# Optimization experiments

Hardware: AMD Instinct MI355X
Metric: run time of the kernel (lower is better)

The kernel has to match this reference:

```python
import jax, jax.numpy as jnp
import numpy as np

B, T, L, A, O = 16, 32, 64, 64, 16
EL, EA, EO = 128, 128, 128
FL, FA, FO, C = 256, 256, 256, 768


def setup_inputs() -> dict:
    key = jax.random.key(0)
    ks = jax.random.split(key, 16)
    s = 0.02
    return {
        "lab_feats": jax.random.normal(ks[0], (B, T, L, FL), jnp.float32),
        "abn_feats": jax.random.normal(ks[1], (B, T, A, FA), jnp.float32),
        "lab_concept_emb": jax.random.normal(ks[2], (L, C), jnp.float32),
        "abn_concept_emb": jax.random.normal(ks[3], (A, C), jnp.float32),
        "lab_rel_emb": jax.random.normal(ks[4], (EL, C), jnp.float32),
        "abn_rel_emb": jax.random.normal(ks[5], (EA, C), jnp.float32),
        "W_lab": jax.random.normal(ks[6], (FL + C, FL), jnp.float32) * s,
        "b_lab": jnp.zeros((FL,), jnp.float32),
        "W_abn": jax.random.normal(ks[7], (FA + C, FA), jnp.float32) * s,
        "b_abn": jnp.zeros((FA,), jnp.float32),
        "W_org": jax.random.normal(ks[8], (FL, FO), jnp.float32) * s,
        "b_org": jnp.zeros((FO,), jnp.float32),
        "D": jax.random.normal(ks[9], (C, FL), jnp.float32) * s,
        "W_o2a": jax.random.normal(ks[10], (FO, FA), jnp.float32) * s,
        "b_o2a": jnp.zeros((FA,), jnp.float32),
        "time_mask": jnp.ones((B, T), dtype=bool),
        "lab_idx": jax.random.randint(ks[11], (EL,), 0, L),
        "lab_org_idx": jax.random.randint(ks[12], (EL,), 0, O),
        "abn_idx": jax.random.randint(ks[13], (EA,), 0, A),
        "abn_org_idx": jax.random.randint(ks[14], (EA,), 0, O),
        "o2a_abn_idx": jax.random.randint(ks[15], (EO,), 0, A),
        "o2a_org_idx": jax.random.randint(jax.random.fold_in(key, 99), (EO,), 0, O),
        "num_organs": O,
    }


def _scatter_mean(attended, org_idx, num_organs, time_mask):
    # attended: (B,T,E,F); emulate legacy per-edge accumulate: cnt[o] = deg(o)*w(b,t)
    onehot = (org_idx[:, None] == jnp.arange(num_organs)[None, :]).astype(attended.dtype)  # (E,O)
    sum_o = jnp.einsum('btef,eo->btof', attended, onehot)
    deg = onehot.sum(0)                                    # (O,)
    w = time_mask.astype(attended.dtype)                   # (B,T)
    cnt = w[:, :, None] * deg[None, None, :]               # (B,T,O)
    mean_o = sum_o / jnp.maximum(cnt, 1e-9)[..., None]
    return mean_o, cnt > 0


def reference(lab_feats, abn_feats, lab_concept_emb, abn_concept_emb,
              lab_rel_emb, abn_rel_emb, W_lab, b_lab, W_abn, b_abn,
              W_org, b_org, D, W_o2a, b_o2a,
              time_mask, lab_idx, lab_org_idx, abn_idx, abn_org_idx,
              o2a_abn_idx, o2a_org_idx, num_organs):
    Fl = lab_feats.shape[-1]
    Fa = abn_feats.shape[-1]
    A_ = abn_feats.shape[2]

    # --- lab -> organ: gather, concat(feat, concept+relation), W_lab (split to avoid concat) ---
    x = lab_feats[:, :, lab_idx, :]                        # (B,T,El,Fl)
    c = lab_concept_emb[lab_idx] + lab_rel_emb             # (El,C)
    h = jnp.tanh(jnp.einsum('btef,fg->bteg', x, W_lab[:Fl]) + c @ W_lab[Fl:] + b_lab)
    attended = h + lab_rel_emb @ D                         # relation-projection D
    mean_lab, mask_lab = _scatter_mean(attended, lab_org_idx, num_organs, time_mask)

    # --- abn -> organ ---
    xa = abn_feats[:, :, abn_idx, :]
    ca = abn_concept_emb[abn_idx] + abn_rel_emb
    ha = jnp.tanh(jnp.einsum('btef,fg->bteg', xa, W_abn[:Fa]) + ca @ W_abn[Fa:] + b_abn)
    mean_abn, mask_abn = _scatter_mean(ha, abn_org_idx, num_organs, time_mask)

    # --- organ states ---
    organ_states = jnp.tanh(jnp.einsum('btof,fg->btog', mean_lab + mean_abn, W_org) + b_org)
    organ_states = organ_states * (mask_lab | mask_abn)[..., None].astype(organ_states.dtype)

    # --- organ -> abnormality message passing (mean over incident organs) ---
    msg = jnp.einsum('btog,gf->btof', organ_states, W_o2a) + b_o2a   # (B,T,O,Fa)
    gathered = msg[:, :, o2a_org_idx, :]                   # (B,T,Eo,Fa)
    onehot = (o2a_abn_idx[:, None] == jnp.arange(A_)[None, :]).astype(msg.dtype)  # (Eo,A)
    agg = jnp.einsum('btef,ea->btaf', gathered, onehot)
    deg = jnp.maximum(onehot.sum(0), 1.0)                  # (A,)
    abn_out = abn_feats + agg / deg[None, None, :, None]
    return abn_out
```

## Files before the change

kernel.cpp:

```cpp
#include <hip/hip_runtime.h>
#include <math.h>

#define NBT 512
#define NF  256
#define NC  768
#define NROW 64
#define NORG 16
#define NE  128
#define SLD 260
#define SY  264

#define WS_SW_LAB1 0
#define WS_SW_ABN1 131072
#define WS_SW_ORG  1441792
#define WS_SW_O2A  1572864
#define WS_SUMREL  1703936
#define WS_LAB_CB  1753088
#define WS_ABN_CB  1884160
#define WS_ADDSUM  2015232
#define WS_WCNT    2031616
#define WS_INVL    2035712
#define WS_INVA    2035776
#define WS_MASK    2035840
#define WS_SRTL    2035904
#define WS_SRTA    2036544
#define WS_RAWL    2097152
#define WS_RAWA    10485760
#define WS_NEED    18874368

typedef __attribute__((ext_vector_type(8)))  short bf16x8;
typedef __attribute__((ext_vector_type(16))) float f32x16;
typedef __attribute__((ext_vector_type(4)))  float f32x4;

__device__ __forceinline__ short f2bf(float f) {
    union { float f; unsigned u; } v; v.f = f;
    unsigned r = v.u + 0x7FFF + ((v.u >> 16) & 1);
    return (short)(r >> 16);
}
__device__ __forceinline__ float bf2f(short s) {
    return __uint_as_float(((unsigned)(unsigned short)s) << 16);
}
__device__ __forceinline__ float tanh_fast(float x) {
    float xc = fminf(fmaxf(x, -15.f), 15.f);
    float e = __expf(2.f * xc);
    return 1.f - 2.f * __builtin_amdgcn_rcpf(e + 1.f);
}
__device__ __forceinline__ f32x16 mfma32(bf16x8 a, bf16x8 b, f32x16 c) {
    return __builtin_amdgcn_mfma_f32_32x32x16_bf16(a, b, c, 0, 0, 0);
}
__device__ __forceinline__ f32x4 mfma16(bf16x8 a, bf16x8 b, f32x4 c) {
    return __builtin_amdgcn_mfma_f32_16x16x32_bf16(a, b, c, 0, 0, 0);
}
__device__ __forceinline__ bf16x8 pack_a16(const float* __restrict__ p) {
    float4 x0 = *(const float4*)p;
    float4 x1 = *(const float4*)(p + 4);
    union { bf16x8 v; unsigned u[4]; } r;
    r.u[0] = __builtin_amdgcn_perm(__float_as_uint(x0.y), __float_as_uint(x0.x), 0x07060302);
    r.u[1] = __builtin_amdgcn_perm(__float_as_uint(x0.w), __float_as_uint(x0.z), 0x07060302);
    r.u[2] = __builtin_amdgcn_perm(__float_as_uint(x1.y), __float_as_uint(x1.x), 0x07060302);
    r.u[3] = __builtin_amdgcn_perm(__float_as_uint(x1.w), __float_as_uint(x1.z), 0x07060302);
    return r.v;
}

__device__ __forceinline__ void swz32(const float* __restrict__ src, short* __restrict__ dst, int s) {
    const int l = s & 63, rest = s >> 6;
    const int nt = rest & 7, k16 = rest >> 3;
    const int n = nt * 32 + (l & 31);
    const int kb = k16 * 16 + ((l >> 5) & 1) * 8;
    bf16x8 v;
    #pragma unroll
    for (int j = 0; j < 8; ++j) v[j] = f2bf(src[(kb + j) * NF + n]);
    *(bf16x8*)(dst + s * 8) = v;
}
__device__ __forceinline__ void swz16(const float* __restrict__ src, short* __restrict__ dst, int s) {
    const int l = s & 63, rest = s >> 6;
    const int nt = rest & 15, k32 = rest >> 4;
    const int n = nt * 16 + (l & 15);
    const int kb = k32 * 32 + ((l >> 4) & 3) * 8;
    bf16x8 v;
    #pragma unroll
    for (int j = 0; j < 8; ++j) v[j] = f2bf(src[(kb + j) * NF + n]);
    *(bf16x8*)(dst + s * 8) = v;
}

__global__ __launch_bounds__(256) void pk_pre2(
    const float* __restrict__ W_lab, const float* __restrict__ W_abn,
    const float* __restrict__ W_org,
    const float* __restrict__ W_o2a, const float* __restrict__ lab_rel,
    const float* __restrict__ lab_con, const float* __restrict__ abn_con,
    const float* __restrict__ abn_rel,
    const float* __restrict__ b_lab, const float* __restrict__ b_abn,
    const int* __restrict__ lab_idx, const int* __restrict__ lab_org_idx,
    const int* __restrict__ abn_idx, const int* __restrict__ abn_org_idx,
    const int* __restrict__ o2a_abn_idx, const int* __restrict__ o2a_org_idx,
    char* __restrict__ ws) {
    __shared__ __align__(16) float sP[4 * 1024];
    const int bid = blockIdx.x;
    if (bid < 64) {
        const int tid = threadIdx.x, l = tid & 63, w = tid >> 6;
        const int side = bid >> 5;
        const int b2 = bid & 31;
        const int mq = b2 >> 3, nb = b2 & 7;
        const int em = mq * 32;
        const float* W2  = side ? (W_abn + NF * NF) : (W_lab + NF * NF);
        const float* con = side ? abn_con : lab_con;
        const float* rel = side ? abn_rel : lab_rel;
        const int*   idx = side ? abn_idx : lab_idx;

        f32x16 acc;
        #pragma unroll
        for (int r = 0; r < 16; ++r) acc[r] = 0.f;

        const int e  = em + (l & 31);
        const int kk = ((l >> 5) & 1) * 8;
        const int n  = nb * 32 + (l & 31);
        const float* cp = con + idx[e] * NC;
        const float* rp = rel + e * NC;
        #pragma unroll 4
        for (int k16 = 0; k16 < 12; ++k16) {
            const int k = (w * 12 + k16) * 16 + kk;
            float4 c0 = *(const float4*)(cp + k);
            float4 c1 = *(const float4*)(cp + k + 4);
            float4 r0 = *(const float4*)(rp + k);
            float4 r1 = *(const float4*)(rp + k + 4);
            float v[8] = {c0.x + r0.x, c0.y + r0.y, c0.z + r0.z, c0.w + r0.w,
                          c1.x + r1.x, c1.y + r1.y, c1.z + r1.z, c1.w + r1.w};
            bf16x8 af;
            #pragma unroll
            for (int j = 0; j < 8; ++j) af[j] = f2bf(v[j]);
            const float* wp = W2 + k * NF + n;
            bf16x8 bv;
            #pragma unroll
            for (int j = 0; j < 8; ++j) bv[j] = f2bf(wp[j * NF]);
            acc = mfma32(af, bv, acc);
        }
        #pragma unroll
        for (int r = 0; r < 16; ++r) sP[w * 1024 + r * 64 + l] = acc[r];
        __syncthreads();
        float* outp = (float*)(ws + (side ? WS_ABN_CB : WS_LAB_CB));
        const float* bias = side ? b_abn : b_lab;
        #pragma unroll
        for (int q = 0; q < 4; ++q) {
            const int idx2 = q * 256 + tid;
            float v = sP[idx2] + sP[1024 + idx2] + sP[2048 + idx2] + sP[3072 + idx2];
            const int reg = idx2 >> 6, ll = idx2 & 63;
            const int er = (reg & 3) + 8 * (reg >> 2) + 4 * (ll >> 5);
            const int col = nb * 32 + (ll & 31);
            outp[(em + er) * NF + col] = v + bias[col];
        }
    } else if (bid < 112) {
        const int b2 = bid - 64;
        const int o = b2 / 3, kth = b2 % 3;
        const int k = kth * 256 + threadIdx.x;
        float s = 0.f;
        #pragma unroll 16
        for (int e = 0; e < NE; ++e) {
            const float v = lab_rel[e * NC + k];
            s += (lab_org_idx[e] == o) ? v : 0.f;
        }
        ((float*)(ws + WS_SUMREL))[o * NC + k] = s;
    } else if (bid == 112) {
        __shared__ int cL[NORG], cA[NORG], cC[NROW * NORG];
        __shared__ int goL[NORG + 1], goA[NORG + 1], curL[NORG], curA[NORG];
        const int t = threadIdx.x;
        for (int i = t; i < NROW * NORG; i += 256) cC[i] = 0;
        if (t < NORG) { cL[t] = 0; cA[t] = 0; }
        __syncthreads();
        if (t < NE) {
            atomicAdd(&cL[lab_org_idx[t]], 1);
            atomicAdd(&cA[abn_org_idx[t]], 1);
            atomicAdd(&cC[o2a_abn_idx[t] * NORG + o2a_org_idx[t]], 1);
        }
        __syncthreads();
        if (t == 0) { int s = 0; for (int o = 0; o < NORG; ++o) { goL[o] = s; s += cL[o]; } goL[NORG] = s; }
        if (t == 1) { int s = 0; for (int o = 0; o < NORG; ++o) { goA[o] = s; s += cA[o]; } goA[NORG] = s; }
        __syncthreads();
        if (t < NORG) { curL[t] = goL[t]; curA[t] = goA[t]; }
        __syncthreads();
        if (t < NE) {
            const int ol = lab_org_idx[t], oa = abn_org_idx[t];
            int p = atomicAdd(&curL[ol], 1);
            ((int*)(ws + WS_SRTL))[p] = (lab_idx[t] << 24) | (ol << 16) | t;
            int q = atomicAdd(&curA[oa], 1);
            ((int*)(ws + WS_SRTA))[q] = (abn_idx[t] << 24) | (oa << 16) | t;
        }
        if (t < NORG) {
            ((float*)(ws + WS_INVL))[t] = cL[t] ? 1.f / (float)cL[t] : 0.f;
            ((float*)(ws + WS_INVA))[t] = cA[t] ? 1.f / (float)cA[t] : 0.f;
            ((float*)(ws + WS_MASK))[t] = (cL[t] || cA[t]) ? 1.f : 0.f;
        }
        if (t < NROW) {
            int dega = 0;
            for (int o = 0; o < NORG; ++o) dega += cC[t * NORG + o];
            float inv = 1.f / (float)(dega > 1 ? dega : 1);
            for (int o = 0; o < NORG; ++o)
                ((float*)(ws + WS_WCNT))[t * NORG + o] = (float)cC[t * NORG + o] * inv;
        }
    } else {
        const int gid = (bid - 113) * 256 + threadIdx.x;
        if      (gid <  8192) swz32(W_lab, (short*)(ws + WS_SW_LAB1), gid);
        else if (gid < 16384) swz32(W_abn, (short*)(ws + WS_SW_ABN1), gid - 8192);
        else if (gid < 24576) swz16(W_org, (short*)(ws + WS_SW_ORG),  gid - 16384);
        else                  swz16(W_o2a, (short*)(ws + WS_SW_O2A),  gid - 24576);
    }
}

__device__ __forceinline__ void stage_A(const float* __restrict__ X, short* __restrict__ sA, int tid) {
    #pragma unroll
    for (int ss = 0; ss < 8; ++ss) {
        const int s = tid + 256 * ss;
        const int k16 = s >> 7, rt = (s >> 6) & 1, l = s & 63;
        const int row = rt * 32 + (l & 31);
        const int kb = k16 * 16 + ((l >> 5) & 1) * 8;
        *(bf16x8*)(sA + s * 8) = pack_a16(X + row * NF + kb);
    }
}

template <int POST>
__device__ __forceinline__ void gemm_small(
    const float* __restrict__ sIn, const short* __restrict__ Bsw,
    const float* __restrict__ bias, const float* __restrict__ mask,
    float* __restrict__ sOut, int tid) {
    const int l = tid & 63, w = tid >> 6;
    f32x4 acc[4];
    #pragma unroll
    for (int i = 0; i < 4; ++i) { acc[i][0] = 0.f; acc[i][1] = 0.f; acc[i][2] = 0.f; acc[i][3] = 0.f; }
    #pragma unroll 2
    for (int k32 = 0; k32 < 8; ++k32) {
        const float* ap = sIn + (l & 15) * SLD + k32 * 32 + ((l >> 4) & 3) * 8;
        bf16x8 af = pack_a16(ap);
        #pragma unroll
        for (int nt = 0; nt < 4; ++nt) {
            bf16x8 bfv = *(const bf16x8*)(Bsw + ((k32 * 16 + w * 4 + nt) * 64 + l) * 8);
            acc[nt] = mfma16(af, bfv, acc[nt]);
        }
    }
    #pragma unroll
    for (int nt = 0; nt < 4; ++nt) {
        const int col = w * 64 + nt * 16 + (l & 15);
        const float b = bias[col];
        #pragma unroll
        for (int reg = 0; reg < 4; ++reg) {
            const int row = ((l >> 4) & 3) * 4 + reg;
            float v = acc[nt][reg] + b;
            if (POST == 0) v = tanh_fast(v) * mask[row];
            sOut[row * SLD + col] = v;
        }
    }
}

__device__ __forceinline__ void addsum_body(const float* __restrict__ D,
                                            char* __restrict__ ws, float* __restrict__ sP,
                                            int nb, int tid) {
    const int l = tid & 63, w = tid >> 6;
    const float* sr = (const float*)(ws + WS_SUMREL);
    f32x16 acc;
    #pragma unroll
    for (int r = 0; r < 16; ++r) acc[r] = 0.f;
    const int row = l & 31;
    const int kk = ((l >> 5) & 1) * 8;
    const int n = nb * 32 + (l & 31);
    const float* cp = sr + row * NC;
    #pragma unroll 4
    for (int k16 = 0; k16 < 12; ++k16) {
        const int k = w * 192 + k16 * 16 + kk;
        bf16x8 af;
        if (row < NORG) {
            af = pack_a16(cp + k);
        } else {
            #pragma unroll
            for (int j = 0; j < 8; ++j) af[j] = 0;
        }
        const float* dp = D + k * NF + n;
        bf16x8 bv;
        #pragma unroll
        for (int j = 0; j < 8; ++j) bv[j] = f2bf(dp[j * NF]);
        acc = mfma32(af, bv, acc);
    }
    #pragma unroll
    for (int r = 0; r < 16; ++r) sP[w * 1024 + r * 64 + l] = acc[r];
    __syncthreads();
    float* outp = (float*)(ws + WS_ADDSUM);
    #pragma unroll
    for (int q = 0; q < 4; ++q) {
        const int idx2 = q * 256 + tid;
        float v = sP[idx2] + sP[1024 + idx2] + sP[2048 + idx2] + sP[3072 + idx2];
        const int reg = idx2 >> 6, ll = idx2 & 63;
        const int er = (reg & 3) + 8 * (reg >> 2) + 4 * (ll >> 5);
        const int col = nb * 32 + (ll & 31);
        if (er < NORG) outp[er * NF + col] = v;
    }
}

__global__ __launch_bounds__(512, 4) void kg_side(
    const float* __restrict__ lab_feats, const float* __restrict__ abn_feats,
    const float* __restrict__ D, char* __restrict__ ws) {
    __shared__ __align__(16) short sY[NROW * SY];
    __shared__ int sE[NE];
    __shared__ float sOv[2 * NF];

    const int tid = threadIdx.x;
    if (blockIdx.x < 8) {
        if (tid < 256) addsum_body(D, ws, (float*)sY, blockIdx.x, tid);
        return;
    }
    const int idx = blockIdx.x - 8;
    const int side = idx >> 9;
    const int bt = idx & 511;

    if (tid < NE) sE[tid] = ((const int*)(ws + (side ? WS_SRTA : WS_SRTL)))[tid];

    const float* X   = (side ? abn_feats : lab_feats) + bt * (NROW * NF);
    const short* Bsw = (const short*)(ws + (side ? WS_SW_ABN1 : WS_SW_LAB1));
    const float* cb  = (const float*)(ws + (side ? WS_ABN_CB : WS_LAB_CB));
    float* rawo = (float*)(ws + (side ? WS_RAWA : WS_RAWL)) + bt * (NORG * NF);

    #pragma unroll
    for (int ss = 0; ss < 4; ++ss) {
        const int s = tid + 512 * ss;
        const int k16 = s >> 7, rt = (s >> 6) & 1, ll = s & 63;
        const int row = rt * 32 + (ll & 31);
        const int kb = k16 * 16 + ((ll >> 5) & 1) * 8;
        *(bf16x8*)(sY + s * 8) = pack_a16(X + row * NF + kb);
    }
    __syncthreads();

    const int l = tid & 63, w = tid >> 6;
    f32x16 acc[2];
    #pragma unroll
    for (int i = 0; i < 2; ++i)
        #pragma unroll
        for (int r = 0; r < 16; ++r) acc[i][r] = 0.f;
    #pragma unroll 8
    for (int k16 = 0; k16 < 16; ++k16) {
        bf16x8 a0 = *(const bf16x8*)(sY + ((k16 * 2 + 0) * 64 + l) * 8);
        bf16x8 a1 = *(const bf16x8*)(sY + ((k16 * 2 + 1) * 64 + l) * 8);
        bf16x8 b0 = *(const bf16x8*)(Bsw + ((k16 * 8 + w) * 64 + l) * 8);
        acc[0] = mfma32(a0, b0, acc[0]);
        acc[1] = mfma32(a1, b0, acc[1]);
    }
    __syncthreads();

    {
        const int col = w * 32 + (l & 31);
        #pragma unroll
        for (int rt = 0; rt < 2; ++rt)
            #pragma unroll
            for (int reg = 0; reg < 16; ++reg) {
                const int row = rt * 32 + (reg & 3) + 8 * (reg >> 2) + 4 * (l >> 5);
                sY[row * SY + col] = f2bf(acc[rt][reg]);
            }
    }
    __syncthreads();

    const int eh = tid >> 8;
    const int t = tid & 255;
    const short* yt = sY + t;
    const float* cbt = cb + t;
    const int ob0 = (__builtin_amdgcn_readfirstlane(sE[63]) >> 16) & 255;
    const int ob1 = (__builtin_amdgcn_readfirstlane(sE[64]) >> 16) & 255;
    const bool bshared = (ob0 == ob1);
    const int ebase = eh * 64;
    float racc = 0.f;
    int curo = (__builtin_amdgcn_readfirstlane(sE[ebase]) >> 16) & 255;
    for (int i0 = 0; i0 < 64; i0 += 8) {
        int   pk8[8];
        float cb8[8], y8[8];
        #pragma unroll
        for (int j = 0; j < 8; ++j) {
            const int pk = __builtin_amdgcn_readfirstlane(sE[ebase + i0 + j]);
            pk8[j] = pk;
            cb8[j] = cbt[(pk & 0xffff) * NF];
            y8[j]  = bf2f(yt[(pk >> 24) * SY]);
        }
        #pragma unroll
        for (int j = 0; j < 8; ++j) {
            const int o = (pk8[j] >> 16) & 255;
            if (o != curo) {
                if (bshared && curo == ob0) sOv[eh * NF + t] = racc;
                else rawo[curo * NF + t] = racc;
                racc = 0.f; curo = o;
            }
            racc += tanh_fast(y8[j] + cb8[j]);
        }
    }
    if (bshared && curo == ob0) sOv[eh * NF + t] = racc;
    else rawo[curo * NF + t] = racc;

    if (bshared) {
        __syncthreads();
        if (tid < NF) rawo[ob0 * NF + tid] = sOv[tid] + sOv[NF + tid];
    }
}

__global__ __launch_bounds__(256, 4) void kg_back(
    const float* __restrict__ abn_feats, const float* __restrict__ b_org,
    const float* __restrict__ b_o2a, const char* __restrict__ ws,
    float* __restrict__ out) {
    __shared__ __align__(16) float sIn[NORG * SLD];
    __shared__ __align__(16) float sSt[NORG * SLD];
    __shared__ float sWc[NROW * NORG];
    __shared__ float sInvL[NORG], sInvA[NORG], sMsk[NORG];

    const int tid = threadIdx.x;
    const int bt = blockIdx.x;

    if      (tid < NORG)     sInvL[tid]          = ((const float*)(ws + WS_INVL))[tid];
    else if (tid < 2 * NORG) sInvA[tid - NORG]   = ((const float*)(ws + WS_INVA))[tid - NORG];
    else if (tid < 3 * NORG) sMsk[tid - 2 * NORG] = ((const float*)(ws + WS_MASK))[tid - 2 * NORG];
    #pragma unroll
    for (int i = tid; i < NROW * NORG; i += 256)
        sWc[i] = ((const float*)(ws + WS_WCNT))[i];

    const float* rawL = (const float*)(ws + WS_RAWL) + bt * (NORG * NF);
    const float* rawA = (const float*)(ws + WS_RAWA) + bt * (NORG * NF);
    const float* addR = (const float*)(ws + WS_ADDSUM);
    __syncthreads();

    const int g = tid;
    #pragma unroll
    for (int o = 0; o < NORG; ++o) {
        const float il = sInvL[o], ia = sInvA[o];
        const float vl = (il > 0.f) ? (rawL[o * NF + g] + addR[o * NF + g]) * il : 0.f;
        const float va = (ia > 0.f) ? rawA[o * NF + g] * ia : 0.f;
        sIn[o * SLD + g] = vl + va;
    }
    __syncthreads();

    gemm_small<0>(sIn, (const short*)(ws + WS_SW_ORG), b_org, sMsk, sSt, tid);
    __syncthreads();
    gemm_small<1>(sSt, (const short*)(ws + WS_SW_O2A), b_o2a, nullptr, sIn, tid);
    __syncthreads();

    float mr[NORG];
    #pragma unroll
    for (int o = 0; o < NORG; ++o) mr[o] = sIn[o * SLD + g];
    const float* src = abn_feats + bt * (NROW * NF);
    float* dst = out + bt * (NROW * NF);
    #pragma unroll 8
    for (int a = 0; a < NROW; ++a) {
        float s = src[a * NF + g];
        #pragma unroll
        for (int o = 0; o < NORG; ++o) s += sWc[a * NORG + o] * mr[o];
        dst[a * NF + g] = s;
    }
}

__global__ __launch_bounds__(256) void pk_addsum(const float* __restrict__ D,
                                                 char* __restrict__ ws) {
    __shared__ __align__(16) float sP[4 * 1024];
    addsum_body(D, ws, sP, blockIdx.x, threadIdx.x);
}

template <bool LAB>
__device__ __forceinline__ void side_pass(
    const float* __restrict__ X, const short* __restrict__ Bsw,
    const float* __restrict__ cb, const float* __restrict__ addR,
    const float* __restrict__ sInv, const int* __restrict__ sE,
    short* __restrict__ sA, float* __restrict__ sAcc, int tid) {
    __syncthreads();
    stage_A(X, sA, tid);
    __syncthreads();
    const int l = tid & 63, w = tid >> 6;
    f32x16 acc[2][2];
    #pragma unroll
    for (int i = 0; i < 2; ++i)
        #pragma unroll
        for (int j = 0; j < 2; ++j)
            #pragma unroll
            for (int r = 0; r < 16; ++r) acc[i][j][r] = 0.f;
    #pragma unroll 8
    for (int k16 = 0; k16 < 16; ++k16) {
        bf16x8 a0 = *(const bf16x8*)(sA + ((k16 * 2 + 0) * 64 + l) * 8);
        bf16x8 a1 = *(const bf16x8*)(sA + ((k16 * 2 + 1) * 64 + l) * 8);
        bf16x8 b0 = *(const bf16x8*)(Bsw + ((k16 * 8 + 2 * w + 0) * 64 + l) * 8);
        bf16x8 b1 = *(const bf16x8*)(Bsw + ((k16 * 8 + 2 * w + 1) * 64 + l) * 8);
        acc[0][0] = mfma32(a0, b0, acc[0][0]);
        acc[1][0] = mfma32(a1, b0, acc[1][0]);
        acc[0][1] = mfma32(a0, b1, acc[0][1]);
        acc[1][1] = mfma32(a1, b1, acc[1][1]);
    }
    __syncthreads();
    short* sYs = sA;
    #pragma unroll
    for (int rt = 0; rt < 2; ++rt)
        #pragma unroll
        for (int nt = 0; nt < 2; ++nt) {
            const int col = w * 64 + nt * 32 + (l & 31);
            #pragma unroll
            for (int reg = 0; reg < 16; ++reg) {
                const int row = rt * 32 + (reg & 3) + 8 * (reg >> 2) + 4 * (l >> 5);
                sYs[row * SY + col] = f2bf(acc[rt][nt][reg]);
            }
        }
    __syncthreads();
    const int t = tid;
    if (LAB) {
        #pragma unroll
        for (int o = 0; o < NORG; ++o)
            sAcc[o * SLD + t] = addR[o * NF + t] * sInv[o];
    }
    float racc = 0.f;
    int curo = (sE[0] >> 16) & 255;
    #pragma unroll 4
    for (int i = 0; i < NE; ++i) {
        const int pk = sE[i];
        const int o = (pk >> 16) & 255;
        if (o != curo) {
            sAcc[curo * SLD + t] += racc * sInv[curo];
            racc = 0.f; curo = o;
        }
        const float yv = bf2f(sYs[(pk >> 24) * SY + t]);
        racc += tanh_fast(yv + cb[(pk & 0xffff) * NF + t]);
    }
    sAcc[curo * SLD + t] += racc * sInv[curo];
}

__global__ __launch_bounds__(256, 2) void kg_main(
    const float* __restrict__ lab_feats, const float* __restrict__ abn_feats,
    const float* __restrict__ b_org, const float* __restrict__ b_o2a,
    const char* __restrict__ ws, float* __restrict__ out) {
    __shared__ __align__(16) short sY[NROW * SY];
    __shared__ __align__(16) float sAcc[NORG * SLD];
    __shared__ __align__(16) float sSt [NORG * SLD];
    __shared__ int   sEL[NE], sEA[NE];
    __shared__ float sInvL[NORG], sInvA[NORG], sMsk[NORG];

    const int tid = threadIdx.x;
    const int bt = blockIdx.x;

    if (tid < NE) {
        sEL[tid] = ((const int*)(ws + WS_SRTL))[tid];
        sEA[tid] = ((const int*)(ws + WS_SRTA))[tid];
    } else {
        const int u = tid - NE;
        if      (u < 16) sInvL[u]      = ((const float*)(ws + WS_INVL))[u];
        else if (u < 32) sInvA[u - 16] = ((const float*)(ws + WS_INVA))[u - 16];
        else if (u < 48) sMsk[u - 32]  = ((const float*)(ws + WS_MASK))[u - 32];
    }

    const float* Xl = lab_feats + bt * (NROW * NF);
    const float* Xa = abn_feats + bt * (NROW * NF);
    side_pass<true >(Xl, (const short*)(ws + WS_SW_LAB1),
                     (const float*)(ws + WS_LAB_CB), (const float*)(ws + WS_ADDSUM),
                     sInvL, sEL, sY, sAcc, tid);
    side_pass<false>(Xa, (const short*)(ws + WS_SW_ABN1),
                     (const float*)(ws + WS_ABN_CB), nullptr,
                     sInvA, sEA, sY, sAcc, tid);
    __syncthreads();

    gemm_small<0>(sAcc, (const short*)(ws + WS_SW_ORG), b_org, sMsk, sSt, tid);
    __syncthreads();
    float* sMsg = sAcc;
    gemm_small<1>(sSt, (const short*)(ws + WS_SW_O2A), b_o2a, nullptr, sMsg, tid);
    __syncthreads();

    {
        const int g = tid;
        float mr[NORG];
        #pragma unroll
        for (int o = 0; o < NORG; ++o) mr[o] = sMsg[o * SLD + g];
        const float* src = abn_feats + bt * (NROW * NF);
        float* dst = out + bt * (NROW * NF);
        const float* wc = (const float*)(ws + WS_WCNT);
        #pragma unroll 4
        for (int a = 0; a < NROW; ++a) {
            float s = src[a * NF + g];
            #pragma unroll
            for (int o = 0; o < NORG; ++o) s += wc[a * NORG + o] * mr[o];
            dst[a * NF + g] = s;
        }
    }
}

extern "C" void kernel_launch(void* const* d_in, const int* in_sizes, int n_in,
                              void* d_out, int out_size, void* d_ws, size_t ws_size,
                              hipStream_t stream) {
    const float* lab_feats   = (const float*)d_in[0];
    const float* abn_feats   = (const float*)d_in[1];
    const float* lab_concept = (const float*)d_in[2];
    const float* abn_concept = (const float*)d_in[3];
    const float* lab_rel     = (const float*)d_in[4];
    const float* abn_rel     = (const float*)d_in[5];
    const float* W_lab       = (const float*)d_in[6];
    const float* b_lab       = (const float*)d_in[7];
    const float* W_abn       = (const float*)d_in[8];
    const float* b_abn       = (const float*)d_in[9];
    const float* W_org       = (const float*)d_in[10];
    const float* b_org       = (const float*)d_in[11];
    const float* D           = (const float*)d_in[12];
    const float* W_o2a       = (const float*)d_in[13];
    const float* b_o2a       = (const float*)d_in[14];
    const int* lab_idx     = (const int*)d_in[16];
    const int* lab_org_idx = (const int*)d_in[17];
    const int* abn_idx     = (const int*)d_in[18];
    const int* abn_org_idx = (const int*)d_in[19];
    const int* o2a_abn_idx = (const int*)d_in[20];
    const int* o2a_org_idx = (const int*)d_in[21];
    char* ws = (char*)d_ws;
    float* out = (float*)d_out;

    pk_pre2<<<241, 256, 0, stream>>>(W_lab, W_abn, W_org, W_o2a, lab_rel,
                                     lab_concept, abn_concept, abn_rel,
                                     b_lab, b_abn,
                                     lab_idx, lab_org_idx, abn_idx, abn_org_idx,
                                     o2a_abn_idx, o2a_org_idx, ws);
    if (ws_size >= (size_t)WS_NEED) {
        kg_side<<<8 + 2 * NBT, 512, 0, stream>>>(lab_feats, abn_feats, D, ws);
        kg_back<<<NBT, 256, 0, stream>>>(abn_feats, b_org, b_o2a, ws, out);
    } else {
        pk_addsum<<<8, 256, 0, stream>>>(D, ws);
        kg_main<<<NBT, 256, 0, stream>>>(lab_feats, abn_feats, b_org, b_o2a, ws, out);
    }
}
```

Measured before the change: 210.4 us.

## Fuse side and back kernels into one per-timestep kernel; fold addsum into preprocessing

Replaces the kg_side and kg_back pair with a single kg_fuse2 kernel per (b,t). That kernel runs both the lab and abn edge passes and accumulates the organ means in shared memory, so the 16 MB raw per-organ intermediates never go to global memory. The relation-sum and its D projection move into pk_pre2 blocks using an LDS-staged bf16 sum, which removes the separate addsum launch. The fused kernel serializes the two sides within a block and halves the grid to 512 blocks, giving less parallelism than the 1024-block side kernel.

```diff
diff --git a/kernel.cpp b/kernel.cpp
--- a/kernel.cpp
+++ b/kernel.cpp
@@ -9,12 +9,12 @@
 #define NE  128
 #define SLD 260
 #define SY  264
+#define SSR 776
 
 #define WS_SW_LAB1 0
 #define WS_SW_ABN1 131072
 #define WS_SW_ORG  1441792
 #define WS_SW_O2A  1572864
-#define WS_SUMREL  1703936
 #define WS_LAB_CB  1753088
 #define WS_ABN_CB  1884160
 #define WS_ADDSUM  2015232
@@ -24,9 +24,7 @@
 #define WS_MASK    2035840
 #define WS_SRTL    2035904
 #define WS_SRTA    2036544
-#define WS_RAWL    2097152
-#define WS_RAWA    10485760
-#define WS_NEED    18874368
+#define WS_NEED    2097152
 
 typedef __attribute__((ext_vector_type(8)))  short bf16x8;
 typedef __attribute__((ext_vector_type(16))) float f32x16;
@@ -86,7 +84,8 @@
 __global__ __launch_bounds__(256) void pk_pre2(
     const float* __restrict__ W_lab, const float* __restrict__ W_abn,
     const float* __restrict__ W_org,
-    const float* __restrict__ W_o2a, const float* __restrict__ lab_rel,
+    const float* __restrict__ W_o2a, const float* __restrict__ D,
+    const float* __restrict__ lab_rel,
     const float* __restrict__ lab_con, const float* __restrict__ abn_con,
     const float* __restrict__ abn_rel,
     const float* __restrict__ b_lab, const float* __restrict__ b_abn,
@@ -95,11 +94,69 @@
     const int* __restrict__ o2a_abn_idx, const int* __restrict__ o2a_org_idx,
     char* __restrict__ ws) {
     __shared__ __align__(16) float sP[4 * 1024];
+    __shared__ __align__(16) short sSR[NORG * SSR];
     const int bid = blockIdx.x;
-    if (bid < 64) {
-        const int tid = threadIdx.x, l = tid & 63, w = tid >> 6;
-        const int side = bid >> 5;
-        const int b2 = bid & 31;
+    const int tid = threadIdx.x;
+    if (bid < 8) {
+        #pragma unroll
+        for (int c = 0; c < 3; ++c) {
+            const int k = c * 256 + tid;
+            float s[16];
+            #pragma unroll
+            for (int o = 0; o < 16; ++o) s[o] = 0.f;
+            #pragma unroll 8
+            for (int e = 0; e < NE; ++e) {
+                const float v = lab_rel[e * NC + k];
+                const int o = lab_org_idx[e];
+                #pragma unroll
+                for (int oo = 0; oo < 16; ++oo) s[oo] += (o == oo) ? v : 0.f;
+            }
+            #pragma unroll
+            for (int o = 0; o < 16; ++o) sSR[o * SSR + k] = f2bf(s[o]);
+        }
+        __syncthreads();
+        const int nb = bid;
+        const int l = tid & 63, w = tid >> 6;
+        f32x16 acc;
+        #pragma unroll
+        for (int r = 0; r < 16; ++r) acc[r] = 0.f;
+        const int row = l & 31;
+        const int kk = ((l >> 5) & 1) * 8;
+        const int n = nb * 32 + (l & 31);
+        #pragma unroll 4
+        for (int k16 = 0; k16 < 12; ++k16) {
+            const int k = w * 192 + k16 * 16 + kk;
+            bf16x8 af;
+            if (row < NORG) {
+                af = *(const bf16x8*)(sSR + row * SSR + k);
+            } else {
+                #pragma unroll
+                for (int j = 0; j < 8; ++j) af[j] = 0;
+            }
+            const float* dp = D + k * NF + n;
+            bf16x8 bv;
+            #pragma unroll
+            for (int j = 0; j < 8; ++j) bv[j] = f2bf(dp[j * NF]);
+            acc = mfma32(af, bv, acc);
+        }
+        #pragma unroll
+        for (int r = 0; r < 16; ++r) sP[w * 1024 + r * 64 + l] = acc[r];
+        __syncthreads();
+        float* outp = (float*)(ws + WS_ADDSUM);
+        #pragma unroll
+        for (int q = 0; q < 4; ++q) {
+            const int idx2 = q * 256 + tid;
+            float v = sP[idx2] + sP[1024 + idx2] + sP[2048 + idx2] + sP[3072 + idx2];
+            const int reg = idx2 >> 6, ll = idx2 & 63;
+            const int er = (reg & 3) + 8 * (reg >> 2) + 4 * (ll >> 5);
+            const int col = nb * 32 + (ll & 31);
+            if (er < NORG) outp[er * NF + col] = v;
+        }
+    } else if (bid < 72) {
+        const int l = tid & 63, w = tid >> 6;
+        const int b = bid - 8;
+        const int side = b >> 5;
+        const int b2 = b & 31;
         const int mq = b2 >> 3, nb = b2 & 7;
         const int em = mq * 32;
         const float* W2  = side ? (W_abn + NF * NF) : (W_lab + NF * NF);
@@ -148,21 +205,10 @@
             const int col = nb * 32 + (ll & 31);
             outp[(em + er) * NF + col] = v + bias[col];
         }
-    } else if (bid < 112) {
-        const int b2 = bid - 64;
-        const int o = b2 / 3, kth = b2 % 3;
-        const int k = kth * 256 + threadIdx.x;
-        float s = 0.f;
-        #pragma unroll 16
-        for (int e = 0; e < NE; ++e) {
-            const float v = lab_rel[e * NC + k];
-            s += (lab_org_idx[e] == o) ? v : 0.f;
-        }
-        ((float*)(ws + WS_SUMREL))[o * NC + k] = s;
-    } else if (bid == 112) {
+    } else if (bid == 72) {
         __shared__ int cL[NORG], cA[NORG], cC[NROW * NORG];
         __shared__ int goL[NORG + 1], goA[NORG + 1], curL[NORG], curA[NORG];
-        const int t = threadIdx.x;
+        const int t = tid;
         for (int i = t; i < NROW * NORG; i += 256) cC[i] = 0;
         if (t < NORG) { cL[t] = 0; cA[t] = 0; }
         __syncthreads();
@@ -197,11 +243,190 @@
                 ((float*)(ws + WS_WCNT))[t * NORG + o] = (float)cC[t * NORG + o] * inv;
         }
     } else {
-        const int gid = (bid - 113) * 256 + threadIdx.x;
+        const int gid = (bid - 73) * 256 + tid;
         if      (gid <  8192) swz32(W_lab, (short*)(ws + WS_SW_LAB1), gid);
         else if (gid < 16384) swz32(W_abn, (short*)(ws + WS_SW_ABN1), gid - 8192);
         else if (gid < 24576) swz16(W_org, (short*)(ws + WS_SW_ORG),  gid - 16384);
         else                  swz16(W_o2a, (short*)(ws + WS_SW_O2A),  gid - 24576);
+    }
+}
+
+template <int POST>
+__device__ __forceinline__ void gemm_small8(
+    const float* __restrict__ sIn, const short* __restrict__ Bsw,
+    const float* __restrict__ bias, const float* __restrict__ mask,
+    float* __restrict__ sOut, int tid) {
+    const int l = tid & 63, w = tid >> 6;
+    f32x4 acc[2];
+    #pragma unroll
+    for (int i = 0; i < 2; ++i) { acc[i][0] = 0.f; acc[i][1] = 0.f; acc[i][2] = 0.f; acc[i][3] = 0.f; }
+    #pragma unroll 2
+    for (int k32 = 0; k32 < 8; ++k32) {
+        const float* ap = sIn + (l & 15) * SLD + k32 * 32 + ((l >> 4) & 3) * 8;
+        bf16x8 af = pack_a16(ap);
+        #pragma unroll
+        for (int nt = 0; nt < 2; ++nt) {
+            bf16x8 bfv = *(const bf16x8*)(Bsw + ((k32 * 16 + w * 2 + nt) * 64 + l) * 8);
+            acc[nt] = mfma16(af, bfv, acc[nt]);
+        }
+    }
+    #pragma unroll
+    for (int nt = 0; nt < 2; ++nt) {
+        const int col = (w * 2 + nt) * 16 + (l & 15);
+        const float b = bias[col];
+        #pragma unroll
+        for (int reg = 0; reg < 4; ++reg) {
+            const int row = ((l >> 4) & 3) * 4 + reg;
+            float v = acc[nt][reg] + b;
+            if (POST == 0) v = tanh_fast(v) * mask[row];
+            sOut[row * SLD + col] = v;
+        }
+    }
+}
+
+__global__ __launch_bounds__(512, 2) void kg_fuse2(
+    const float* __restrict__ lab_feats, const float* __restrict__ abn_feats,
+    const float* __restrict__ b_org, const float* __restrict__ b_o2a,
+    const char* __restrict__ ws, float* __restrict__ out) {
+    __shared__ __align__(16) short sY[NROW * SY];
+    __shared__ __align__(16) float sAcc[NORG * SLD];
+    __shared__ float sWc[NROW * NORG];
+    __shared__ int sEL[NE], sEA[NE];
+    __shared__ float sOv[2 * NF];
+    __shared__ float sInvL[NORG], sInvA[NORG], sMsk[NORG];
+
+    const int tid = threadIdx.x;
+    const int bt = blockIdx.x;
+
+    if (tid < NE)          sEL[tid]      = ((const int*)(ws + WS_SRTL))[tid];
+    else if (tid < 2 * NE) sEA[tid - NE] = ((const int*)(ws + WS_SRTA))[tid - NE];
+    else {
+        const int u = tid - 2 * NE;
+        if      (u < 16) sInvL[u]       = ((const float*)(ws + WS_INVL))[u];
+        else if (u < 32) sInvA[u - 16]  = ((const float*)(ws + WS_INVA))[u - 16];
+        else if (u < 48) sMsk[u - 32]   = ((const float*)(ws + WS_MASK))[u - 32];
+    }
+    #pragma unroll
+    for (int i = tid; i < NROW * NORG; i += 512)
+        sWc[i] = ((const float*)(ws + WS_WCNT))[i];
+    #pragma unroll
+    for (int i = tid; i < NORG * NF; i += 512)
+        sAcc[(i >> 8) * SLD + (i & 255)] = 0.f;
+
+    const float* addR = (const float*)(ws + WS_ADDSUM);
+    const int l = tid & 63, w = tid >> 6;
+
+    for (int side = 0; side < 2; ++side) {
+        const float* X   = (side ? abn_feats : lab_feats) + bt * (NROW * NF);
+        const short* Bsw = (const short*)(ws + (side ? WS_SW_ABN1 : WS_SW_LAB1));
+        const float* cb  = (const float*)(ws + (side ? WS_ABN_CB : WS_LAB_CB));
+        const int* sE    = side ? sEA : sEL;
+
+        __syncthreads();
+        #pragma unroll
+        for (int ss = 0; ss < 4; ++ss) {
+            const int s = tid + 512 * ss;
+            const int k16 = s >> 7, rt = (s >> 6) & 1, ll = s & 63;
+            const int row = rt * 32 + (ll & 31);
+            const int kb = k16 * 16 + ((ll >> 5) & 1) * 8;
+            *(bf16x8*)(sY + s * 8) = pack_a16(X + row * NF + kb);
+        }
+        __syncthreads();
+        f32x16 acc[2];
+        #pragma unroll
+        for (int i = 0; i < 2; ++i)
+            #pragma unroll
+            for (int r = 0; r < 16; ++r) acc[i][r] = 0.f;
+        #pragma unroll 8
+        for (int k16 = 0; k16 < 16; ++k16) {
+            bf16x8 a0 = *(const bf16x8*)(sY + ((k16 * 2 + 0) * 64 + l) * 8);
+            bf16x8 a1 = *(const bf16x8*)(sY + ((k16 * 2 + 1) * 64 + l) * 8);
+            bf16x8 b0 = *(const bf16x8*)(Bsw + ((k16 * 8 + w) * 64 + l) * 8);
+            acc[0] = mfma32(a0, b0, acc[0]);
+            acc[1] = mfma32(a1, b0, acc[1]);
+        }
+        __syncthreads();
+        {
+            const int col = w * 32 + (l & 31);
+            #pragma unroll
+            for (int rt = 0; rt < 2; ++rt)
+                #pragma unroll
+                for (int reg = 0; reg < 16; ++reg) {
+                    const int row = rt * 32 + (reg & 3) + 8 * (reg >> 2) + 4 * (l >> 5);
+                    sY[row * SY + col] = f2bf(acc[rt][reg]);
+                }
+        }
+        __syncthreads();
+
+        const int eh = tid >> 8;
+        const int t = tid & 255;
+        const short* yt = sY + t;
+        const float* cbt = cb + t;
+        const int ob0 = (__builtin_amdgcn_readfirstlane(sE[63]) >> 16) & 255;
+        const int ob1 = (__builtin_amdgcn_readfirstlane(sE[64]) >> 16) & 255;
+        const bool bshared = (ob0 == ob1);
+        const int ebase = eh * 64;
+        float racc = 0.f;
+        int curo = (__builtin_amdgcn_readfirstlane(sE[ebase]) >> 16) & 255;
+        for (int i0 = 0; i0 < 64; i0 += 8) {
+            int   pk8[8];
+            float cb8[8], y8[8];
+            #pragma unroll
+            for (int j = 0; j < 8; ++j) {
+                const int pk = __builtin_amdgcn_readfirstlane(sE[ebase + i0 + j]);
+                pk8[j] = pk;
+                cb8[j] = cbt[(pk & 0xffff) * NF];
+                y8[j]  = bf2f(yt[(pk >> 24) * SY]);
+            }
+            #pragma unroll
+            for (int j = 0; j < 8; ++j) {
+                const int o = (pk8[j] >> 16) & 255;
+                if (o != curo) {
+                    if (bshared && curo == ob0) sOv[eh * NF + t] = racc;
+                    else if (side == 0) sAcc[curo * SLD + t] = (racc + addR[curo * NF + t]) * sInvL[curo];
+                    else                sAcc[curo * SLD + t] += racc * sInvA[curo];
+                    racc = 0.f; curo = o;
+                }
+                racc += tanh_fast(y8[j] + cb8[j]);
+            }
+        }
+        if (bshared && curo == ob0) sOv[eh * NF + t] = racc;
+        else if (side == 0) sAcc[curo * SLD + t] = (racc + addR[curo * NF + t]) * sInvL[curo];
+        else                sAcc[curo * SLD + t] += racc * sInvA[curo];
+
+        if (bshared) {
+            __syncthreads();
+            if (tid < NF) {
+                const float v = sOv[tid] + sOv[NF + tid];
+                if (side == 0) sAcc[ob0 * SLD + tid] = (v + addR[ob0 * NF + tid]) * sInvL[ob0];
+                else           sAcc[ob0 * SLD + tid] += v * sInvA[ob0];
+            }
+        }
+    }
+    __syncthreads();
+
+    float* sSt  = (float*)sY;
+    float* sMsg = (float*)sY + NORG * SLD;
+    gemm_small8<0>(sAcc, (const short*)(ws + WS_SW_ORG), b_org, sMsk, sSt, tid);
+    __syncthreads();
+    gemm_small8<1>(sSt, (const short*)(ws + WS_SW_O2A), b_o2a, nullptr, sMsg, tid);
+    __syncthreads();
+
+    {
+        const int t = tid & 255, rh = tid >> 8;
+        float mr[NORG];
+        #pragma unroll
+        for (int o = 0; o < NORG; ++o) mr[o] = sMsg[o * SLD + t];
+        const float* src = abn_feats + bt * (NROW * NF);
+        float* dst = out + bt * (NROW * NF);
+        #pragma unroll 8
+        for (int a0 = 0; a0 < 32; ++a0) {
+            const int a = rh * 32 + a0;
+            float s = src[a * NF + t];
+            #pragma unroll
+            for (int o = 0; o < NORG; ++o) s += sWc[a * NORG + o] * mr[o];
+            dst[a * NF + t] = s;
+        }
     }
 }
 
@@ -247,209 +472,6 @@
             sOut[row * SLD + col] = v;
         }
     }
-}
-
-__device__ __forceinline__ void addsum_body(const float* __restrict__ D,
-                                            char* __restrict__ ws, float* __restrict__ sP,
-                                            int nb, int tid) {
-    const int l = tid & 63, w = tid >> 6;
-    const float* sr = (const float*)(ws + WS_SUMREL);
-    f32x16 acc;
-    #pragma unroll
-    for (int r = 0; r < 16; ++r) acc[r] = 0.f;
-    const int row = l & 31;
-    const int kk = ((l >> 5) & 1) * 8;
-    const int n = nb * 32 + (l & 31);
-    const float* cp = sr + row * NC;
-    #pragma unroll 4
-    for (int k16 = 0; k16 < 12; ++k16) {
-        const int k = w * 192 + k16 * 16 + kk;
-        bf16x8 af;
-        if (row < NORG) {
-            af = pack_a16(cp + k);
-        } else {
-            #pragma unroll
-            for (int j = 0; j < 8; ++j) af[j] = 0;
-        }
-        const float* dp = D + k * NF + n;
-        bf16x8 bv;
-        #pragma unroll
-        for (int j = 0; j < 8; ++j) bv[j] = f2bf(dp[j * NF]);
-        acc = mfma32(af, bv, acc);
-    }
-    #pragma unroll
-    for (int r = 0; r < 16; ++r) sP[w * 1024 + r * 64 + l] = acc[r];
-    __syncthreads();
-    float* outp = (float*)(ws + WS_ADDSUM);
-    #pragma unroll
-    for (int q = 0; q < 4; ++q) {
-        const int idx2 = q * 256 + tid;
-        float v = sP[idx2] + sP[1024 + idx2] + sP[2048 + idx2] + sP[3072 + idx2];
-        const int reg = idx2 >> 6, ll = idx2 & 63;
-        const int er = (reg & 3) + 8 * (reg >> 2) + 4 * (ll >> 5);
-        const int col = nb * 32 + (ll & 31);
-        if (er < NORG) outp[er * NF + col] = v;
-    }
-}
-
-__global__ __launch_bounds__(512, 4) void kg_side(
-    const float* __restrict__ lab_feats, const float* __restrict__ abn_feats,
-    const float* __restrict__ D, char* __restrict__ ws) {
-    __shared__ __align__(16) short sY[NROW * SY];
-    __shared__ int sE[NE];
-    __shared__ float sOv[2 * NF];
-
-    const int tid = threadIdx.x;
-    if (blockIdx.x < 8) {
-        if (tid < 256) addsum_body(D, ws, (float*)sY, blockIdx.x, tid);
-        return;
-    }
-    const int idx = blockIdx.x - 8;
-    const int side = idx >> 9;
-    const int bt = idx & 511;
-
-    if (tid < NE) sE[tid] = ((const int*)(ws + (side ? WS_SRTA : WS_SRTL)))[tid];
-
-    const float* X   = (side ? abn_feats : lab_feats) + bt * (NROW * NF);
-    const short* Bsw = (const short*)(ws + (side ? WS_SW_ABN1 : WS_SW_LAB1));
-    const float* cb  = (const float*)(ws + (side ? WS_ABN_CB : WS_LAB_CB));
-    float* rawo = (float*)(ws + (side ? WS_RAWA : WS_RAWL)) + bt * (NORG * NF);
-
-    #pragma unroll
-    for (int ss = 0; ss < 4; ++ss) {
-        const int s = tid + 512 * ss;
-        const int k16 = s >> 7, rt = (s >> 6) & 1, ll = s & 63;
-        const int row = rt * 32 + (ll & 31);
-        const int kb = k16 * 16 + ((ll >> 5) & 1) * 8;
-        *(bf16x8*)(sY + s * 8) = pack_a16(X + row * NF + kb);
-    }
-    __syncthreads();
-
-    const int l = tid & 63, w = tid >> 6;
-    f32x16 acc[2];
-    #pragma unroll
-    for (int i = 0; i < 2; ++i)
-        #pragma unroll
-        for (int r = 0; r < 16; ++r) acc[i][r] = 0.f;
-    #pragma unroll 8
-    for (int k16 = 0; k16 < 16; ++k16) {
-        bf16x8 a0 = *(const bf16x8*)(sY + ((k16 * 2 + 0) * 64 + l) * 8);
-        bf16x8 a1 = *(const bf16x8*)(sY + ((k16 * 2 + 1) * 64 + l) * 8);
-        bf16x8 b0 = *(const bf16x8*)(Bsw + ((k16 * 8 + w) * 64 + l) * 8);
-        acc[0] = mfma32(a0, b0, acc[0]);
-        acc[1] = mfma32(a1, b0, acc[1]);
-    }
-    __syncthreads();
-
-    {
-        const int col = w * 32 + (l & 31);
-        #pragma unroll
-        for (int rt = 0; rt < 2; ++rt)
-            #pragma unroll
-            for (int reg = 0; reg < 16; ++reg) {
-                const int row = rt * 32 + (reg & 3) + 8 * (reg >> 2) + 4 * (l >> 5);
-                sY[row * SY + col] = f2bf(acc[rt][reg]);
-            }
-    }
-    __syncthreads();
-
-    const int eh = tid >> 8;
-    const int t = tid & 255;
-    const short* yt = sY + t;
-    const float* cbt = cb + t;
-    const int ob0 = (__builtin_amdgcn_readfirstlane(sE[63]) >> 16) & 255;
-    const int ob1 = (__builtin_amdgcn_readfirstlane(sE[64]) >> 16) & 255;
-    const bool bshared = (ob0 == ob1);
-    const int ebase = eh * 64;
-    float racc = 0.f;
-    int curo = (__builtin_amdgcn_readfirstlane(sE[ebase]) >> 16) & 255;
-    for (int i0 = 0; i0 < 64; i0 += 8) {
-        int   pk8[8];
-        float cb8[8], y8[8];
-        #pragma unroll
-        for (int j = 0; j < 8; ++j) {
-            const int pk = __builtin_amdgcn_readfirstlane(sE[ebase + i0 + j]);
-            pk8[j] = pk;
-            cb8[j] = cbt[(pk & 0xffff) * NF];
-            y8[j]  = bf2f(yt[(pk >> 24) * SY]);
-        }
-        #pragma unroll
-        for (int j = 0; j < 8; ++j) {
-            const int o = (pk8[j] >> 16) & 255;
-            if (o != curo) {
-                if (bshared && curo == ob0) sOv[eh * NF + t] = racc;
-                else rawo[curo * NF + t] = racc;
-                racc = 0.f; curo = o;
-            }
-            racc += tanh_fast(y8[j] + cb8[j]);
-        }
-    }
-    if (bshared && curo == ob0) sOv[eh * NF + t] = racc;
-    else rawo[curo * NF + t] = racc;
-
-    if (bshared) {
-        __syncthreads();
-        if (tid < NF) rawo[ob0 * NF + tid] = sOv[tid] + sOv[NF + tid];
-    }
-}
-
-__global__ __launch_bounds__(256, 4) void kg_back(
-    const float* __restrict__ abn_feats, const float* __restrict__ b_org,
-    const float* __restrict__ b_o2a, const char* __restrict__ ws,
-    float* __restrict__ out) {
-    __shared__ __align__(16) float sIn[NORG * SLD];
-    __shared__ __align__(16) float sSt[NORG * SLD];
-    __shared__ float sWc[NROW * NORG];
-    __shared__ float sInvL[NORG], sInvA[NORG], sMsk[NORG];
-
-    const int tid = threadIdx.x;
-    const int bt = blockIdx.x;
-
-    if      (tid < NORG)     sInvL[tid]          = ((const float*)(ws + WS_INVL))[tid];
-    else if (tid < 2 * NORG) sInvA[tid - NORG]   = ((const float*)(ws + WS_INVA))[tid - NORG];
-    else if (tid < 3 * NORG) sMsk[tid - 2 * NORG] = ((const float*)(ws + WS_MASK))[tid - 2 * NORG];
-    #pragma unroll
-    for (int i = tid; i < NROW * NORG; i += 256)
-        sWc[i] = ((const float*)(ws + WS_WCNT))[i];
-
-    const float* rawL = (const float*)(ws + WS_RAWL) + bt * (NORG * NF);
-    const float* rawA = (const float*)(ws + WS_RAWA) + bt * (NORG * NF);
-    const float* addR = (const float*)(ws + WS_ADDSUM);
-    __syncthreads();
-
-    const int g = tid;
-    #pragma unroll
-    for (int o = 0; o < NORG; ++o) {
-        const float il = sInvL[o], ia = sInvA[o];
-        const float vl = (il > 0.f) ? (rawL[o * NF + g] + addR[o * NF + g]) * il : 0.f;
-        const float va = (ia > 0.f) ? rawA[o * NF + g] * ia : 0.f;
-        sIn[o * SLD + g] = vl + va;
-    }
-    __syncthreads();
-
-    gemm_small<0>(sIn, (const short*)(ws + WS_SW_ORG), b_org, sMsk, sSt, tid);
-    __syncthreads();
-    gemm_small<1>(sSt, (const short*)(ws + WS_SW_O2A), b_o2a, nullptr, sIn, tid);
-    __syncthreads();
-
-    float mr[NORG];
-    #pragma unroll
-    for (int o = 0; o < NORG; ++o) mr[o] = sIn[o * SLD + g];
-    const float* src = abn_feats + bt * (NROW * NF);
-    float* dst = out + bt * (NROW * NF);
-    #pragma unroll 8
-    for (int a = 0; a < NROW; ++a) {
-        float s = src[a * NF + g];
-        #pragma unroll
-        for (int o = 0; o < NORG; ++o) s += sWc[a * NORG + o] * mr[o];
-        dst[a * NF + g] = s;
-    }
-}
-
-__global__ __launch_bounds__(256) void pk_addsum(const float* __restrict__ D,
-                                                 char* __restrict__ ws) {
-    __shared__ __align__(16) float sP[4 * 1024];
-    addsum_body(D, ws, sP, blockIdx.x, threadIdx.x);
 }
 
 template <bool LAB>
@@ -600,16 +622,14 @@
     char* ws = (char*)d_ws;
     float* out = (float*)d_out;
 
-    pk_pre2<<<241, 256, 0, stream>>>(W_lab, W_abn, W_org, W_o2a, lab_rel,
+    pk_pre2<<<201, 256, 0, stream>>>(W_lab, W_abn, W_org, W_o2a, D, lab_rel,
                                      lab_concept, abn_concept, abn_rel,
                                      b_lab, b_abn,
                                      lab_idx, lab_org_idx, abn_idx, abn_org_idx,
                                      o2a_abn_idx, o2a_org_idx, ws);
     if (ws_size >= (size_t)WS_NEED) {
-        kg_side<<<8 + 2 * NBT, 512, 0, stream>>>(lab_feats, abn_feats, D, ws);
-        kg_back<<<NBT, 256, 0, stream>>>(abn_feats, b_org, b_o2a, ws, out);
+        kg_fuse2<<<NBT, 512, 0, stream>>>(lab_feats, abn_feats, b_org, b_o2a, ws, out);
     } else {
-        pk_addsum<<<8, 256, 0, stream>>>(D, ws);
         kg_main<<<NBT, 256, 0, stream>>>(lab_feats, abn_feats, b_org, b_o2a, ws, out);
     }
 }
```

Result: slower. 234.0 us (+11.2%).
